# Performance work log

Hardware: AMD Instinct MI355X
Metric: run time of the kernel (lower is better)

The kernel has to match this reference:

```python
import jax, jax.numpy as jnp
import numpy as np

B, L, D, T = 8, 4096, 2048, 128  # batch, seq len, hidden dim, max num targets
LN_EPS = 1e-5


def setup_inputs() -> dict:
    key = jax.random.key(0)
    ks = jax.random.split(key, 6)
    context_repr = jax.random.normal(ks[0], (B, L, D), dtype=jnp.float32)
    # varying target counts per row, max exactly T (so num_targets == T as in torch)
    counts = np.minimum((np.arange(B) * 41 + 7) % (T + 1), T)
    counts[0] = T
    counts = jnp.asarray(counts, dtype=jnp.int32)
    pos = jnp.arange(L)
    target_mask = (pos[None, :] < counts[:, None]).astype(jnp.float32)  # [B,L]
    context_mask = 1.0 - target_mask  # valid context = non-target positions
    s1 = 1.0 / np.sqrt(D)
    s2 = 1.0 / np.sqrt(2 * D)
    W1 = jax.random.uniform(ks[1], (D, 2 * D), jnp.float32, -s1, s1)
    b1 = jax.random.uniform(ks[2], (2 * D,), jnp.float32, -s1, s1)
    gamma = jnp.ones((2 * D,), jnp.float32)
    beta = jnp.zeros((2 * D,), jnp.float32)
    W2 = jax.random.uniform(ks[3], (2 * D, D), jnp.float32, -s2, s2)
    b2 = jax.random.uniform(ks[4], (D,), jnp.float32, -s2, s2)
    return {
        "context_repr": context_repr,
        "target_mask": target_mask,
        "context_mask": context_mask,
        "W1": W1, "b1": b1, "gamma": gamma, "beta": beta, "W2": W2, "b2": b2,
        "num_targets": T,
    }


def reference(context_repr, target_mask, context_mask, W1, b1, gamma, beta, W2, b2, num_targets):
    # masked mean pool: sum over ALL positions (targets assumed zeroed),
    # divide by number of valid context positions (faithful to torch code)
    ctx_count = context_mask.sum(axis=-1)                     # [B]
    ctx_sum = context_repr.sum(axis=1)                        # [B,D]
    mean = ctx_sum / jnp.maximum(ctx_count, 1.0)[:, None]
    mean = jnp.where((ctx_count > 0)[:, None], mean, 0.0)     # [B,D]
    # MLP: Linear -> GELU(exact) -> LayerNorm -> Linear
    h = jax.nn.gelu(mean @ W1 + b1, approximate=False)        # [B,2D]
    mu = h.mean(axis=-1, keepdims=True)
    var = jnp.mean((h - mu) ** 2, axis=-1, keepdims=True)
    hn = (h - mu) * jax.lax.rsqrt(var + LN_EPS) * gamma + beta
    out = hn @ W2 + b2                                        # [B,D]
    # scatter prediction into first num_tgt slots per row, rest zeros
    tgt_counts = target_mask.sum(axis=-1)                     # [B]
    valid = jnp.arange(num_targets)[None, :] < tgt_counts[:, None]  # [B,T]
    return jnp.where(valid[:, :, None], out[:, None, :], 0.0)  # [B,T,D]
```

## Files before the change

kernel.cpp:

```cpp
#include <hip/hip_runtime.h>
#include <math.h>

#define B_    8
#define L_    4096
#define D_    2048
#define D2_   4096
#define T_    128
#define LN_EPS_ 1e-5f

#define NLC    32
#define LCHUNK (L_ / NLC)
#define KC1    64
#define NK1    (D_ / KC1)
#define KC2    64
#define NK2    (D2_ / KC2)

__global__ void k_masks(const float* __restrict__ tmask,
                        const float* __restrict__ cmask,
                        float* __restrict__ cnt, float* __restrict__ tcnt) {
  const int b = blockIdx.x;
  const int tid = threadIdx.x;
  float sc = 0.f, st = 0.f;
  for (int i = tid * 4; i < L_; i += 256 * 4) {
    const float4 c4 = *reinterpret_cast<const float4*>(cmask + b * L_ + i);
    const float4 t4 = *reinterpret_cast<const float4*>(tmask + b * L_ + i);
    sc += c4.x + c4.y + c4.z + c4.w;
    st += t4.x + t4.y + t4.z + t4.w;
  }
  __shared__ float sC[256], sT[256];
  sC[tid] = sc; sT[tid] = st;
  __syncthreads();
  for (int off = 128; off > 0; off >>= 1) {
    if (tid < off) { sC[tid] += sC[tid + off]; sT[tid] += sT[tid + off]; }
    __syncthreads();
  }
  if (tid == 0) { cnt[b] = sC[0]; tcnt[b] = sT[0]; }
}

__global__ void k_pool(const float* __restrict__ x, float* __restrict__ part) {
  const int lc = blockIdx.x;
  const int db = blockIdx.y;
  const int b  = blockIdx.z;
  const int d  = db * 1024 + threadIdx.x * 4;
  const float* p = x + (size_t)b * L_ * D_ + (size_t)lc * LCHUNK * D_ + d;
  float ax = 0.f, ay = 0.f, az = 0.f, aw = 0.f;
  #pragma unroll 16
  for (int l = 0; l < LCHUNK; ++l) {
    const float4 v = *reinterpret_cast<const float4*>(p + (size_t)l * D_);
    ax += v.x; ay += v.y; az += v.z; aw += v.w;
  }
  float4 o = make_float4(ax, ay, az, aw);
  *reinterpret_cast<float4*>(part + ((size_t)lc * B_ + b) * D_ + d) = o;
}

__global__ void k_gemv1(const float* __restrict__ part_pool,
                        const float* __restrict__ W1,
                        float* __restrict__ part1) {
  const int j  = blockIdx.x * 256 + threadIdx.x;
  const int ky = blockIdx.y;
  const int k0 = ky * KC1;
  __shared__ float s[B_][KC1];
  for (int i = threadIdx.x; i < B_ * KC1; i += 256) {
    const int bb = i / KC1, kk = i % KC1;
    float v = 0.f;
    #pragma unroll 8
    for (int lc = 0; lc < NLC; ++lc)
      v += part_pool[((size_t)lc * B_ + bb) * D_ + k0 + kk];
    s[bb][kk] = v;
  }
  __syncthreads();
  float acc[B_];
  #pragma unroll
  for (int bb = 0; bb < B_; ++bb) acc[bb] = 0.f;
  const float* w = W1 + (size_t)k0 * D2_ + j;
  #pragma unroll 4
  for (int k = 0; k < KC1; ++k) {
    const float wv = w[(size_t)k * D2_];
    #pragma unroll
    for (int bb = 0; bb < B_; ++bb) acc[bb] += s[bb][k] * wv;
  }
  #pragma unroll
  for (int bb = 0; bb < B_; ++bb)
    part1[((size_t)ky * B_ + bb) * D2_ + j] = acc[bb];
}

__global__ void k_gelu_ln(const float* __restrict__ part1,
                          const float* __restrict__ cnt,
                          const float* __restrict__ b1,
                          const float* __restrict__ gamma,
                          const float* __restrict__ beta,
                          float* __restrict__ hn) {
  const int b = blockIdx.x;
  const int tid = threadIdx.x;
  const float c = cnt[b];
  const float scale = (c > 0.f) ? (1.f / fmaxf(c, 1.f)) : 0.f;
  const int j = tid * 4;
  float hx = 0.f, hy = 0.f, hz = 0.f, hw = 0.f;
  #pragma unroll 8
  for (int ky = 0; ky < NK1; ++ky) {
    const float4 v = *reinterpret_cast<const float4*>(
        part1 + ((size_t)ky * B_ + b) * D2_ + j);
    hx += v.x; hy += v.y; hz += v.z; hw += v.w;
  }
  const float4 bb = *reinterpret_cast<const float4*>(b1 + j);
  float g[4];
  {
    const float v0 = hx * scale + bb.x;
    const float v1 = hy * scale + bb.y;
    const float v2 = hz * scale + bb.z;
    const float v3 = hw * scale + bb.w;
    g[0] = 0.5f * v0 * (1.f + erff(v0 * 0.70710678118654752f));
    g[1] = 0.5f * v1 * (1.f + erff(v1 * 0.70710678118654752f));
    g[2] = 0.5f * v2 * (1.f + erff(v2 * 0.70710678118654752f));
    g[3] = 0.5f * v3 * (1.f + erff(v3 * 0.70710678118654752f));
  }
  float lsum = g[0] + g[1] + g[2] + g[3];
  float lsq  = g[0]*g[0] + g[1]*g[1] + g[2]*g[2] + g[3]*g[3];
  __shared__ float sS[1024], sQ[1024];
  sS[tid] = lsum; sQ[tid] = lsq;
  __syncthreads();
  for (int off = 512; off > 0; off >>= 1) {
    if (tid < off) { sS[tid] += sS[tid + off]; sQ[tid] += sQ[tid + off]; }
    __syncthreads();
  }
  const float mu  = sS[0] * (1.f / D2_);
  const float var = sQ[0] * (1.f / D2_) - mu * mu;
  const float rs  = rsqrtf(var + LN_EPS_);
  const float4 gm = *reinterpret_cast<const float4*>(gamma + j);
  const float4 bt = *reinterpret_cast<const float4*>(beta + j);
  float4 o;
  o.x = (g[0] - mu) * rs * gm.x + bt.x;
  o.y = (g[1] - mu) * rs * gm.y + bt.y;
  o.z = (g[2] - mu) * rs * gm.z + bt.z;
  o.w = (g[3] - mu) * rs * gm.w + bt.w;
  *reinterpret_cast<float4*>(hn + (size_t)b * D2_ + j) = o;
}

__global__ void k_gemv2(const float* __restrict__ HN,
                        const float* __restrict__ W2,
                        float* __restrict__ part2) {
  const int d  = blockIdx.x * 256 + threadIdx.x;
  const int ky = blockIdx.y;
  const int j0 = ky * KC2;
  __shared__ float s[B_][KC2];
  for (int i = threadIdx.x; i < B_ * KC2; i += 256) {
    const int bb = i / KC2, jj = i % KC2;
    s[bb][jj] = HN[bb * D2_ + j0 + jj];
  }
  __syncthreads();
  float acc[B_];
  #pragma unroll
  for (int bb = 0; bb < B_; ++bb) acc[bb] = 0.f;
  const float* w = W2 + (size_t)j0 * D_ + d;
  #pragma unroll 4
  for (int k = 0; k < KC2; ++k) {
    const float wv = w[(size_t)k * D_];
    #pragma unroll
    for (int bb = 0; bb < B_; ++bb) acc[bb] += s[bb][k] * wv;
  }
  #pragma unroll
  for (int bb = 0; bb < B_; ++bb)
    part2[((size_t)ky * B_ + bb) * D_ + d] = acc[bb];
}

__global__ void k_reduce2(const float* __restrict__ part2,
                          const float* __restrict__ b2,
                          float* __restrict__ out_pre) {
  const int idx = (blockIdx.x * 256 + threadIdx.x) * 4;
  const int b = idx / D_;
  const int d = idx % D_;
  float ax = 0.f, ay = 0.f, az = 0.f, aw = 0.f;
  #pragma unroll 8
  for (int ky = 0; ky < NK2; ++ky) {
    const float4 v = *reinterpret_cast<const float4*>(
        part2 + ((size_t)ky * B_ + b) * D_ + d);
    ax += v.x; ay += v.y; az += v.z; aw += v.w;
  }
  const float4 bv = *reinterpret_cast<const float4*>(b2 + d);
  *reinterpret_cast<float4*>(out_pre + idx) =
      make_float4(ax + bv.x, ay + bv.y, az + bv.z, aw + bv.w);
}

__global__ void k_scatter(const float* __restrict__ out_pre,
                          const float* __restrict__ tcnt,
                          float* __restrict__ out) {
  const size_t idx = ((size_t)blockIdx.x * 256 + threadIdx.x) * 4;
  const int d  = (int)(idx % D_);
  const int bt = (int)(idx / D_);
  const int t  = bt % T_;
  const int b  = bt / T_;
  float4 v = make_float4(0.f, 0.f, 0.f, 0.f);
  if (t < (int)(tcnt[b] + 0.5f)) {
    v = *reinterpret_cast<const float4*>(out_pre + b * D_ + d);
  }
  *reinterpret_cast<float4*>(out + idx) = v;
}

extern "C" void kernel_launch(void* const* d_in, const int* in_sizes, int n_in,
                              void* d_out, int out_size, void* d_ws, size_t ws_size,
                              hipStream_t stream) {
  const float* context_repr = (const float*)d_in[0];
  const float* target_mask  = (const float*)d_in[1];
  const float* context_mask = (const float*)d_in[2];
  const float* W1    = (const float*)d_in[3];
  const float* b1    = (const float*)d_in[4];
  const float* gamma = (const float*)d_in[5];
  const float* beta  = (const float*)d_in[6];
  const float* W2    = (const float*)d_in[7];
  const float* b2    = (const float*)d_in[8];
  float* out = (float*)d_out;

  float* ws        = (float*)d_ws;
  float* part_pool = ws;
  float* cnt       = part_pool + (size_t)NLC * B_ * D_;
  float* tcnt      = cnt + B_;
  float* part1     = tcnt + B_;
  float* hn        = part1 + (size_t)NK1 * B_ * D2_;
  float* part2     = hn + (size_t)B_ * D2_;
  float* out_pre   = part2 + (size_t)NK2 * B_ * D_;

  k_masks<<<dim3(B_), dim3(256), 0, stream>>>(target_mask, context_mask, cnt, tcnt);

  k_pool<<<dim3(NLC, 2, B_), dim3(256), 0, stream>>>(context_repr, part_pool);

  k_gemv1<<<dim3(D2_ / 256, NK1), dim3(256), 0, stream>>>(part_pool, W1, part1);

  k_gelu_ln<<<dim3(B_), dim3(1024), 0, stream>>>(part1, cnt, b1, gamma, beta, hn);

  k_gemv2<<<dim3(D_ / 256, NK2), dim3(256), 0, stream>>>(hn, W2, part2);

  k_reduce2<<<dim3((B_ * D_) / 1024), dim3(256), 0, stream>>>(part2, b2, out_pre);

  const int n_out4 = out_size / 4;
  k_scatter<<<dim3((n_out4 + 255) / 256), dim3(256), 0, stream>>>(out_pre, tcnt, out);
}
```

Before: 447.2 us.

## Fuse mask counting into pooling, vectorize GEMVs, merge reduce and scatter

Folds the mask-count kernel into the pooling launch as an extra block column, and merges the final reduction with the target scatter into one output kernel. Both GEMVs now use float4 weight loads with four outputs per thread. Their K-chunks shrink from 64 to 16, and the pooling L-split doubles to 64. The aim is fewer launches, no intermediate out_pre buffer, and wider loads. The cost is that the partial buffers grow about fourfold. Those buffers are reduced by only 8 LayerNorm blocks and 16 output blocks, and those 16 blocks also write the full output serially.

```diff
diff --git a/kernel.cpp b/kernel.cpp
--- a/kernel.cpp
+++ b/kernel.cpp
@@ -8,88 +8,99 @@
 #define T_    128
 #define LN_EPS_ 1e-5f
 
-#define NLC    32
+#define NLC    64
 #define LCHUNK (L_ / NLC)
-#define KC1    64
+#define KC1    16
 #define NK1    (D_ / KC1)
-#define KC2    64
+#define KC2    16
 #define NK2    (D2_ / KC2)
 
-__global__ void k_masks(const float* __restrict__ tmask,
-                        const float* __restrict__ cmask,
-                        float* __restrict__ cnt, float* __restrict__ tcnt) {
-  const int b = blockIdx.x;
-  const int tid = threadIdx.x;
-  float sc = 0.f, st = 0.f;
-  for (int i = tid * 4; i < L_; i += 256 * 4) {
-    const float4 c4 = *reinterpret_cast<const float4*>(cmask + b * L_ + i);
-    const float4 t4 = *reinterpret_cast<const float4*>(tmask + b * L_ + i);
-    sc += c4.x + c4.y + c4.z + c4.w;
-    st += t4.x + t4.y + t4.z + t4.w;
-  }
-  __shared__ float sC[256], sT[256];
-  sC[tid] = sc; sT[tid] = st;
-  __syncthreads();
-  for (int off = 128; off > 0; off >>= 1) {
-    if (tid < off) { sC[tid] += sC[tid + off]; sT[tid] += sT[tid + off]; }
-    __syncthreads();
-  }
-  if (tid == 0) { cnt[b] = sC[0]; tcnt[b] = sT[0]; }
-}
-
-__global__ void k_pool(const float* __restrict__ x, float* __restrict__ part) {
+__global__ __launch_bounds__(256)
+void k_pool_masks(const float* __restrict__ x,
+                  const float* __restrict__ tmask,
+                  const float* __restrict__ cmask,
+                  float* __restrict__ part,
+                  float* __restrict__ cnt, float* __restrict__ tcnt) {
   const int lc = blockIdx.x;
   const int db = blockIdx.y;
   const int b  = blockIdx.z;
-  const int d  = db * 1024 + threadIdx.x * 4;
-  const float* p = x + (size_t)b * L_ * D_ + (size_t)lc * LCHUNK * D_ + d;
+  const int tid = threadIdx.x;
+
+  if (lc == NLC) {
+    if (db != 0) return;
+    float sc = 0.f, st = 0.f;
+    for (int i = tid * 4; i < L_; i += 256 * 4) {
+      const float4 c4 = *reinterpret_cast<const float4*>(cmask + b * L_ + i);
+      const float4 t4 = *reinterpret_cast<const float4*>(tmask + b * L_ + i);
+      sc += c4.x + c4.y + c4.z + c4.w;
+      st += t4.x + t4.y + t4.z + t4.w;
+    }
+    __shared__ float sC[256], sT[256];
+    sC[tid] = sc; sT[tid] = st;
+    __syncthreads();
+    for (int off = 128; off > 0; off >>= 1) {
+      if (tid < off) { sC[tid] += sC[tid + off]; sT[tid] += sT[tid + off]; }
+      __syncthreads();
+    }
+    if (tid == 0) { cnt[b] = sC[0]; tcnt[b] = sT[0]; }
+    return;
+  }
+
+  const int d  = db * 1024 + tid * 4;
+  const float* p = x + ((size_t)b * L_ + (size_t)lc * LCHUNK) * D_ + d;
   float ax = 0.f, ay = 0.f, az = 0.f, aw = 0.f;
   #pragma unroll 16
   for (int l = 0; l < LCHUNK; ++l) {
     const float4 v = *reinterpret_cast<const float4*>(p + (size_t)l * D_);
     ax += v.x; ay += v.y; az += v.z; aw += v.w;
   }
-  float4 o = make_float4(ax, ay, az, aw);
-  *reinterpret_cast<float4*>(part + ((size_t)lc * B_ + b) * D_ + d) = o;
-}
-
-__global__ void k_gemv1(const float* __restrict__ part_pool,
-                        const float* __restrict__ W1,
-                        float* __restrict__ part1) {
-  const int j  = blockIdx.x * 256 + threadIdx.x;
+  *reinterpret_cast<float4*>(part + ((size_t)lc * B_ + b) * D_ + d) =
+      make_float4(ax, ay, az, aw);
+}
+
+__global__ __launch_bounds__(256)
+void k_gemv1(const float* __restrict__ part_pool,
+             const float* __restrict__ W1,
+             float* __restrict__ part1) {
+  const int j  = blockIdx.x * 1024 + threadIdx.x * 4;
   const int ky = blockIdx.y;
   const int k0 = ky * KC1;
   __shared__ float s[B_][KC1];
   for (int i = threadIdx.x; i < B_ * KC1; i += 256) {
-    const int bb = i / KC1, kk = i % KC1;
+    const int bb = i >> 4, kk = i & (KC1 - 1);
+    const float* pp = part_pool + (size_t)bb * D_ + k0 + kk;
     float v = 0.f;
-    #pragma unroll 8
-    for (int lc = 0; lc < NLC; ++lc)
-      v += part_pool[((size_t)lc * B_ + bb) * D_ + k0 + kk];
+    #pragma unroll 16
+    for (int lc = 0; lc < NLC; ++lc) v += pp[(size_t)lc * B_ * D_];
     s[bb][kk] = v;
   }
   __syncthreads();
-  float acc[B_];
-  #pragma unroll
-  for (int bb = 0; bb < B_; ++bb) acc[bb] = 0.f;
+  float4 acc[B_];
+  #pragma unroll
+  for (int bb = 0; bb < B_; ++bb) acc[bb] = make_float4(0.f, 0.f, 0.f, 0.f);
   const float* w = W1 + (size_t)k0 * D2_ + j;
-  #pragma unroll 4
+  #pragma unroll
   for (int k = 0; k < KC1; ++k) {
-    const float wv = w[(size_t)k * D2_];
+    const float4 wv = *reinterpret_cast<const float4*>(w + (size_t)k * D2_);
     #pragma unroll
-    for (int bb = 0; bb < B_; ++bb) acc[bb] += s[bb][k] * wv;
+    for (int bb = 0; bb < B_; ++bb) {
+      const float sv = s[bb][k];
+      acc[bb].x += sv * wv.x; acc[bb].y += sv * wv.y;
+      acc[bb].z += sv * wv.z; acc[bb].w += sv * wv.w;
+    }
   }
   #pragma unroll
   for (int bb = 0; bb < B_; ++bb)
-    part1[((size_t)ky * B_ + bb) * D2_ + j] = acc[bb];
-}
-
-__global__ void k_gelu_ln(const float* __restrict__ part1,
-                          const float* __restrict__ cnt,
-                          const float* __restrict__ b1,
-                          const float* __restrict__ gamma,
-                          const float* __restrict__ beta,
-                          float* __restrict__ hn) {
+    *reinterpret_cast<float4*>(part1 + ((size_t)ky * B_ + bb) * D2_ + j) = acc[bb];
+}
+
+__global__ __launch_bounds__(1024)
+void k_gelu_ln(const float* __restrict__ part1,
+               const float* __restrict__ cnt,
+               const float* __restrict__ b1,
+               const float* __restrict__ gamma,
+               const float* __restrict__ beta,
+               float* __restrict__ hn) {
   const int b = blockIdx.x;
   const int tid = threadIdx.x;
   const float c = cnt[b];
@@ -136,39 +147,46 @@
   *reinterpret_cast<float4*>(hn + (size_t)b * D2_ + j) = o;
 }
 
-__global__ void k_gemv2(const float* __restrict__ HN,
-                        const float* __restrict__ W2,
-                        float* __restrict__ part2) {
-  const int d  = blockIdx.x * 256 + threadIdx.x;
+__global__ __launch_bounds__(256)
+void k_gemv2(const float* __restrict__ HN,
+             const float* __restrict__ W2,
+             float* __restrict__ part2) {
+  const int d  = blockIdx.x * 1024 + threadIdx.x * 4;
   const int ky = blockIdx.y;
   const int j0 = ky * KC2;
   __shared__ float s[B_][KC2];
   for (int i = threadIdx.x; i < B_ * KC2; i += 256) {
-    const int bb = i / KC2, jj = i % KC2;
-    s[bb][jj] = HN[bb * D2_ + j0 + jj];
+    const int bb = i >> 4, jj = i & (KC2 - 1);
+    s[bb][jj] = HN[(size_t)bb * D2_ + j0 + jj];
   }
   __syncthreads();
-  float acc[B_];
-  #pragma unroll
-  for (int bb = 0; bb < B_; ++bb) acc[bb] = 0.f;
+  float4 acc[B_];
+  #pragma unroll
+  for (int bb = 0; bb < B_; ++bb) acc[bb] = make_float4(0.f, 0.f, 0.f, 0.f);
   const float* w = W2 + (size_t)j0 * D_ + d;
-  #pragma unroll 4
+  #pragma unroll
   for (int k = 0; k < KC2; ++k) {
-    const float wv = w[(size_t)k * D_];
+    const float4 wv = *reinterpret_cast<const float4*>(w + (size_t)k * D_);
     #pragma unroll
-    for (int bb = 0; bb < B_; ++bb) acc[bb] += s[bb][k] * wv;
+    for (int bb = 0; bb < B_; ++bb) {
+      const float sv = s[bb][k];
+      acc[bb].x += sv * wv.x; acc[bb].y += sv * wv.y;
+      acc[bb].z += sv * wv.z; acc[bb].w += sv * wv.w;
+    }
   }
   #pragma unroll
   for (int bb = 0; bb < B_; ++bb)
-    part2[((size_t)ky * B_ + bb) * D_ + d] = acc[bb];
-}
-
-__global__ void k_reduce2(const float* __restrict__ part2,
-                          const float* __restrict__ b2,
-                          float* __restrict__ out_pre) {
-  const int idx = (blockIdx.x * 256 + threadIdx.x) * 4;
-  const int b = idx / D_;
-  const int d = idx % D_;
+    *reinterpret_cast<float4*>(part2 + ((size_t)ky * B_ + bb) * D_ + d) = acc[bb];
+}
+
+__global__ __launch_bounds__(256)
+void k_out(const float* __restrict__ part2,
+           const float* __restrict__ b2,
+           const float* __restrict__ tcnt,
+           float* __restrict__ out) {
+  const int b    = blockIdx.x >> 1;
+  const int half = blockIdx.x & 1;
+  const int d    = half * 1024 + threadIdx.x * 4;
   float ax = 0.f, ay = 0.f, az = 0.f, aw = 0.f;
   #pragma unroll 8
   for (int ky = 0; ky < NK2; ++ky) {
@@ -177,23 +195,12 @@
     ax += v.x; ay += v.y; az += v.z; aw += v.w;
   }
   const float4 bv = *reinterpret_cast<const float4*>(b2 + d);
-  *reinterpret_cast<float4*>(out_pre + idx) =
-      make_float4(ax + bv.x, ay + bv.y, az + bv.z, aw + bv.w);
-}
-
-__global__ void k_scatter(const float* __restrict__ out_pre,
-                          const float* __restrict__ tcnt,
-                          float* __restrict__ out) {
-  const size_t idx = ((size_t)blockIdx.x * 256 + threadIdx.x) * 4;
-  const int d  = (int)(idx % D_);
-  const int bt = (int)(idx / D_);
-  const int t  = bt % T_;
-  const int b  = bt / T_;
-  float4 v = make_float4(0.f, 0.f, 0.f, 0.f);
-  if (t < (int)(tcnt[b] + 0.5f)) {
-    v = *reinterpret_cast<const float4*>(out_pre + b * D_ + d);
-  }
-  *reinterpret_cast<float4*>(out + idx) = v;
+  const float4 val = make_float4(ax + bv.x, ay + bv.y, az + bv.z, aw + bv.w);
+  const float4 zero = make_float4(0.f, 0.f, 0.f, 0.f);
+  const int tc = (int)(tcnt[b] + 0.5f);
+  float* o = out + ((size_t)b * T_) * D_ + d;
+  for (int t = 0; t < T_; ++t)
+    *reinterpret_cast<float4*>(o + (size_t)t * D_) = (t < tc) ? val : zero;
 }
 
 extern "C" void kernel_launch(void* const* d_in, const int* in_sizes, int n_in,
@@ -217,20 +224,15 @@
   float* part1     = tcnt + B_;
   float* hn        = part1 + (size_t)NK1 * B_ * D2_;
   float* part2     = hn + (size_t)B_ * D2_;
-  float* out_pre   = part2 + (size_t)NK2 * B_ * D_;
-
-  k_masks<<<dim3(B_), dim3(256), 0, stream>>>(target_mask, context_mask, cnt, tcnt);
-
-  k_pool<<<dim3(NLC, 2, B_), dim3(256), 0, stream>>>(context_repr, part_pool);
-
-  k_gemv1<<<dim3(D2_ / 256, NK1), dim3(256), 0, stream>>>(part_pool, W1, part1);
+
+  k_pool_masks<<<dim3(NLC + 1, 2, B_), dim3(256), 0, stream>>>(
+      context_repr, target_mask, context_mask, part_pool, cnt, tcnt);
+
+  k_gemv1<<<dim3(4, NK1), dim3(256), 0, stream>>>(part_pool, W1, part1);
 
   k_gelu_ln<<<dim3(B_), dim3(1024), 0, stream>>>(part1, cnt, b1, gamma, beta, hn);
 
-  k_gemv2<<<dim3(D_ / 256, NK2), dim3(256), 0, stream>>>(hn, W2, part2);
-
-  k_reduce2<<<dim3((B_ * D_) / 1024), dim3(256), 0, stream>>>(part2, b2, out_pre);
-
-  const int n_out4 = out_size / 4;
-  k_scatter<<<dim3((n_out4 + 255) / 256), dim3(256), 0, stream>>>(out_pre, tcnt, out);
-}
+  k_gemv2<<<dim3(2, NK2), dim3(256), 0, stream>>>(hn, W2, part2);
+
+  k_out<<<dim3(2 * B_), dim3(256), 0, stream>>>(part2, b2, tcnt, out);
+}
```

Result: slower. 480.5 us (+7.4%).
